# Performance work log

Measured on AMD Instinct MI355X. Metric: run time of the kernel, lower is better.

## Reference

```python
import jax, jax.numpy as jnp
import numpy as np

B, N = 4, 256
EDGE_F = 256; NODE_F = 256; MSG = 128; LINK_H = 128
ROUNDS = 3; CLASSES = 600


def setup_inputs() -> dict:
    key = jax.random.key(0)
    ks = jax.random.split(key, 16)
    s = 0.05
    return {
        "edge_features": jax.random.normal(ks[0], (B, N, N, EDGE_F), jnp.float32),
        "node_features": jax.random.normal(ks[1], (B, N, NODE_F), jnp.float32),
        "adj_mat": jnp.zeros((B, N, N), jnp.float32),
        "node_labels": jnp.zeros((B, N, CLASSES), jnp.float32),
        "human_nums": jax.random.randint(ks[2], (B,), 0, 16),
        "obj_nums": jax.random.randint(ks[3], (B,), 0, 224),
        # feature-resize linears
        "W_er": jax.random.normal(ks[4], (EDGE_F, MSG), jnp.float32) * s,
        "b_er": jnp.zeros((MSG,), jnp.float32),
        "W_nr": jax.random.normal(ks[5], (NODE_F, MSG), jnp.float32) * s,
        "b_nr": jnp.zeros((MSG,), jnp.float32),
        # link function: 1x1 GraphConv stack MSG -> LINK_H -> 1
        "W_l1": jax.random.normal(ks[6], (MSG, LINK_H), jnp.float32) * s,
        "b_l1": jnp.zeros((LINK_H,), jnp.float32),
        "W_l2": jax.random.normal(ks[7], (LINK_H, 1), jnp.float32) * s,
        "b_l2": jnp.zeros((1,), jnp.float32),
        # message function: linear_concat_relu  (cat(h_w, e_vw) -> MSG)
        "W_msg": jax.random.normal(ks[8], (2 * MSG, MSG), jnp.float32) * s,
        "b_msg": jnp.zeros((MSG,), jnp.float32),
        # GRU update (torch gate order r,z,n)
        "W_ih": jax.random.normal(ks[9], (MSG, 3 * MSG), jnp.float32) * s,
        "b_ih": jnp.zeros((3 * MSG,), jnp.float32),
        "W_hh": jax.random.normal(ks[10], (MSG, 3 * MSG), jnp.float32) * s,
        "b_hh": jnp.zeros((3 * MSG,), jnp.float32),
        # readout fc
        "W_ro": jax.random.normal(ks[11], (MSG, CLASSES), jnp.float32) * s,
        "b_ro": jnp.zeros((CLASSES,), jnp.float32),
    }


def _gru_cell(x, h, W_ih, b_ih, W_hh, b_hh):
    gi = x @ W_ih + b_ih
    gh = h @ W_hh + b_hh
    ir, iz, i_n = jnp.split(gi, 3, axis=-1)
    hr, hz, h_n = jnp.split(gh, 3, axis=-1)
    r = jax.nn.sigmoid(ir + hr)
    z = jax.nn.sigmoid(iz + hz)
    n = jnp.tanh(i_n + r * h_n)
    return (1.0 - z) * n + z * h


def reference(edge_features, node_features, adj_mat, node_labels,
              human_nums, obj_nums,
              W_er, b_er, W_nr, b_nr, W_l1, b_l1, W_l2, b_l2,
              W_msg, b_msg, W_ih, b_ih, W_hh, b_hh, W_ro, b_ro):
    Bn, Nn = node_features.shape[0], node_features.shape[1]
    # resize_feature_to_message_size
    ef = edge_features @ W_er + b_er          # [B, N(i=receiver), N(w=sender), M]
    nf = node_features @ W_nr + b_nr          # [B, N, M]

    valid = (human_nums + obj_nums).astype(jnp.int32)
    node_mask = (jnp.arange(Nn)[None, :] < valid[:, None]).astype(ef.dtype)  # [B,N]
    pair_mask = node_mask[:, :, None] * node_mask[:, None, :]                # [B,N,N]

    # NOTE: the original forward never writes updated node states back into
    # hidden_node_states, so every round uses the ORIGINAL (resized) node and
    # edge features for the message function -> m_raw is round-invariant.
    cat = jnp.concatenate(
        [jnp.broadcast_to(nf[:, None, :, :], ef.shape), ef], axis=-1)  # [B,N,N,2M]
    m_raw = jax.nn.relu(cat @ W_msg + b_msg)                           # [B,N,N,M]

    e_state = ef                                    # hidden edge state, round 0
    pred_adj = jnp.zeros((Bn, Nn, Nn), ef.dtype)
    pred_labels = jnp.zeros((Bn, Nn, CLASSES), ef.dtype)
    for rnd in range(ROUNDS):
        # GraphConv link function (1x1 convs == per-edge MLP), valid block only
        hlink = jax.nn.relu(e_state @ W_l1 + b_l1)
        pred_adj = pair_mask * (hlink @ W_l2 + b_l2)[..., 0]     # [B,N,N]
        gate = jax.nn.sigmoid(pred_adj) * node_mask[:, None, :]  # zero invalid senders
        m = gate[..., None] * m_raw                              # [B,N,N,M]
        # next-round hidden edge state: column i holds gated messages to node i
        e_state = jnp.where(pair_mask[..., None] > 0, jnp.swapaxes(m, 1, 2), ef)
        if rnd == ROUNDS - 1:
            m_sum = m.sum(axis=2)                                # [B,N,M]
            h_new = _gru_cell(m_sum, nf, W_ih, b_ih, W_hh, b_hh)
            pred_labels = node_mask[..., None] * (h_new @ W_ro + b_ro)
    return pred_adj, pred_labels
```

## Files before the change

kernel.cpp:

```cpp
#include <hip/hip_runtime.h>
#include <hip/hip_bf16.h>


#define B_ 4
#define N_ 256
#define EF_ 256
#define M_ 128
#define CL_ 600
#define ADJ_SZ (B_*N_*N_)

typedef __hip_bfloat16 bf16;
typedef short short8 __attribute__((ext_vector_type(8)));
typedef float f32x4 __attribute__((ext_vector_type(4)));

#define MFMA(a,b,c) __builtin_amdgcn_mfma_f32_16x16x32_bf16(a,b,c,0,0,0)

__device__ __forceinline__ float s2f(short s){
  union { unsigned int u; float f; } x; x.u = ((unsigned int)(unsigned short)s) << 16; return x.f;
}
__device__ __forceinline__ bf16 f2b(float f){ return __float2bfloat16(f); }
__device__ __forceinline__ short f2bs(float f){
  bf16 h = __float2bfloat16(f);
  return *reinterpret_cast<short*>(&h);
}
__device__ __forceinline__ float sigm(float x){ return 1.0f/(1.0f+expf(-x)); }

template<bool BF> __device__ __forceinline__ float ld(const void* p, size_t i){
  if (BF) return s2f(((const short*)p)[i]);
  return ((const float*)p)[i];
}
template<bool BF> __device__ __forceinline__ void st(void* p, size_t i, float v){
  if (BF) ((bf16*)p)[i] = f2b(v);
  else    ((float*)p)[i] = v;
}
__device__ __forceinline__ float dot8(short8 w, const float* x){
  float a = 0.f;
  #pragma unroll
  for (int j=0;j<8;j++) a += x[j]*s2f(w[j]);
  return a;
}

__global__ __launch_bounds__(64)
void k_detect(const unsigned short* ef, int* flag){
  int t = threadIdx.x;
  int cnt = 0;
  for (int j = 0; j < 64; j++){
    unsigned short u = ef[t*64 + j];
    int e = (u >> 7) & 0xFF;
    cnt += (e >= 96 && e <= 144) ? 1 : 0;
  }
  for (int o = 32; o > 0; o >>= 1) cnt += __shfl_down(cnt, o, 64);
  if (t == 0) *flag = (cnt > 3500) ? 1 : 0;
}

template<bool BF>
__global__ __launch_bounds__(256)
void k_zero(void* out, int n, const int* dflag){
  if ((*dflag != 0) != BF) return;
  int i = blockIdx.x*256 + threadIdx.x;
  if (i < n) st<BF>(out, i, 0.0f);
}

template<bool BF>
__global__ __launch_bounds__(64)
void k_pack(const void* src, int K, int N, bf16* dst, const int* dflag){
  if ((*dflag != 0) != BF) return;
  int blk = blockIdx.x;
  int n16 = N >> 4;
  int kk = blk / n16, nt = blk % n16;
  int lane = threadIdx.x;
  int k0 = kk*32 + (lane>>4)*8;
  int n  = nt*16 + (lane&15);
  size_t dbase = ((size_t)blk*64 + lane)*8;
  #pragma unroll
  for (int j=0;j<8;j++)
    dst[dbase+j] = f2b(ld<BF>(src, (size_t)(k0+j)*N + n));
}

template<bool BF>
__global__ __launch_bounds__(256)
void k_tr(const void* src, int K, int N, bf16* dst, const int* dflag){
  if ((*dflag != 0) != BF) return;
  int idx = blockIdx.x*256 + threadIdx.x;
  if (idx >= K*N) return;
  int k = idx / N, n = idx % N;
  dst[(size_t)n*K + k] = f2b(ld<BF>(src, idx));
}

template<bool BF>
__global__ __launch_bounds__(128)
void k_nf_c(const void* nodef, const bf16* tWnr, const void* b_nr,
            const bf16* tWmsgT, const void* b_msg, float* nf, float* cb,
            const int* dflag)
{
  if ((*dflag != 0) != BF) return;
  int blk = blockIdx.x; int b = blk >> 8; int v = blk & 255;
  int t = threadIdx.x;
  __shared__ float xs[EF_];
  __shared__ float nfs[M_];
  size_t xrow = ((size_t)(b*N_)+v)*EF_;
  xs[t]     = ld<BF>(nodef, xrow + t);
  xs[t+128] = ld<BF>(nodef, xrow + t + 128);
  __syncthreads();
  float acc = ld<BF>(b_nr, t);
  const short8* wp = (const short8*)(tWnr + (size_t)t*EF_);
  #pragma unroll 4
  for (int k8=0;k8<32;k8++) acc += dot8(wp[k8], &xs[k8*8]);
  nf[((size_t)(b*N_)+v)*M_+t] = acc;
  nfs[t] = acc;
  __syncthreads();
  float acc2 = ld<BF>(b_msg, t);
  const short8* wq = (const short8*)(tWmsgT + (size_t)t*M_);
  #pragma unroll 4
  for (int k8=0;k8<16;k8++) acc2 += dot8(wq[k8], &nfs[k8*8]);
  cb[((size_t)(b*N_)+v)*M_+t] = acc2;
}

template<bool BF>
__global__ __launch_bounds__(256)
void k_r0(const void* edgef, const bf16* pWer, const void* b_er,
          const bf16* pWmsgB, const float* cb, const bf16* pWl1,
          const void* b_l1, const void* W_l2, const void* b_l2,
          const int* hn, const int* on, bf16* mraw, float* s0,
          const int* dflag)
{
  if ((*dflag != 0) != BF) return;
  int b = blockIdx.z, i = blockIdx.y, w0 = blockIdx.x*32;
  int valid = hn[b] + on[b];
  if (i >= valid || w0 >= valid) return;
  int t = threadIdx.x;
  __shared__ __attribute__((aligned(16))) bf16 EfsB[32][136];
  __shared__ __attribute__((aligned(16))) char uni[32*264*2];
  bf16  (*Xs)[264]  = (bf16(*)[264])uni;
  float (*hls)[132] = (float(*)[132])uni;

  {
    int j = t>>3, c = (t&7)*32;
    size_t g = (((size_t)(b*N_)+i)*N_ + (size_t)(w0+j))*EF_ + c;
    if (BF){
      const short8* src = (const short8*)((const short*)edgef + g);
      short8* dst = (short8*)&Xs[j][c];
      #pragma unroll
      for (int u=0;u<4;u++) dst[u] = src[u];
    } else {
      const float* src = (const float*)edgef + g;
      #pragma unroll
      for (int u=0;u<32;u++) Xs[j][c+u] = f2b(src[u]);
    }
  }
  __syncthreads();

  int lane = t & 63, wv = t >> 6;
  int r0 = (wv&1)*16;
  int c0h = wv >> 1;
  int mA = r0 + (lane&15);
  int kq = (lane>>4)*8;
  int qrow = r0 + (lane>>4)*4;

  f32x4 z4 = {0.f,0.f,0.f,0.f};
  f32x4 acc[4] = {z4,z4,z4,z4};
  for (int kk=0;kk<8;kk++){
    short8 a = *(const short8*)&Xs[mA][kk*32 + kq];
    #pragma unroll
    for (int nt=0;nt<4;nt++){
      int gnt = c0h*4 + nt;
      short8 bb = *(const short8*)(pWer + (((size_t)kk*8 + gnt)*64 + lane)*8);
      acc[nt] = MFMA(a, bb, acc[nt]);
    }
  }
  #pragma unroll
  for (int nt=0;nt<4;nt++){
    int col = c0h*64 + nt*16 + (lane&15);
    float be = ld<BF>(b_er, col);
    #pragma unroll
    for (int r=0;r<4;r++)
      EfsB[qrow+r][col] = f2b(acc[nt][r] + be);
  }
  __syncthreads();

  f32x4 am[4] = {z4,z4,z4,z4};
  f32x4 ah[4] = {z4,z4,z4,z4};
  for (int kk=0;kk<4;kk++){
    short8 a = *(const short8*)&EfsB[mA][kk*32 + kq];
    #pragma unroll
    for (int nt=0;nt<4;nt++){
      int gnt = c0h*4 + nt;
      size_t off = (((size_t)kk*8 + gnt)*64 + lane)*8;
      short8 b1 = *(const short8*)(pWmsgB + off);
      am[nt] = MFMA(a, b1, am[nt]);
      short8 b2 = *(const short8*)(pWl1 + off);
      ah[nt] = MFMA(a, b2, ah[nt]);
    }
  }
  #pragma unroll
  for (int nt=0;nt<4;nt++){
    int col = c0h*64 + nt*16 + (lane&15);
    float bl = ld<BF>(b_l1, col);
    #pragma unroll
    for (int r=0;r<4;r++){
      int row = qrow + r;
      int w = w0 + row;
      float v = am[nt][r] + cb[((size_t)(b*N_)+w)*M_ + col];
      mraw[(((size_t)(b*N_)+i)*N_ + w)*M_ + col] = f2b(fmaxf(v, 0.f));
      hls[row][col] = fmaxf(ah[nt][r] + bl, 0.f);
    }
  }
  __syncthreads();
  {
    int row = t>>3, seg = t&7;
    float p = 0.f;
    #pragma unroll
    for (int k=0;k<16;k++) p += hls[row][seg*16+k] * ld<BF>(W_l2, seg*16+k);
    p += __shfl_down(p, 4, 8);
    p += __shfl_down(p, 2, 8);
    p += __shfl_down(p, 1, 8);
    if (seg==0 && (w0+row) < valid)
      s0[((size_t)(b*N_)+i)*N_ + w0 + row] = p + ld<BF>(b_l2, 0);
  }
}

template<bool BF>
__global__ __launch_bounds__(256)
void k_link2(const bf16* mraw, const float* s_prev, const bf16* pWl1,
             const void* b_l1, const void* W_l2, const void* b_l2,
             const int* hn, const int* on, float* s_next, const int* dflag)
{
  if ((*dflag != 0) != BF) return;
  int b = blockIdx.z, i = blockIdx.y, w0 = blockIdx.x*32;
  int valid = hn[b] + on[b];
  if (i >= valid || w0 >= valid) return;
  int t = threadIdx.x;
  __shared__ __attribute__((aligned(16))) bf16 EsB[32][136];
  __shared__ __attribute__((aligned(16))) float hls[32][132];
  __shared__ float sg[32];
  if (t < 32){
    int w = w0 + t;
    sg[t] = (w < valid) ? sigm(s_prev[((size_t)(b*N_)+w)*N_ + i]) : 0.f;
  }
  __syncthreads();
  {
    int j = t>>3, c = (t&7)*16;
    const short* src = (const short*)mraw + (((size_t)(b*N_)+(size_t)(w0+j))*N_ + i)*M_;
    float s = sg[j];
    #pragma unroll
    for (int u=0;u<2;u++){
      short8 v = *(const short8*)(src + c + u*8);
      short8 o;
      #pragma unroll
      for (int e=0;e<8;e++) o[e] = f2bs(s2f(v[e])*s);
      *(short8*)&EsB[j][c+u*8] = o;
    }
  }
  __syncthreads();

  int lane = t & 63, wv = t >> 6;
  int r0 = (wv&1)*16;
  int c0h = wv >> 1;
  int mA = r0 + (lane&15);
  int kq = (lane>>4)*8;
  int qrow = r0 + (lane>>4)*4;

  f32x4 z4 = {0.f,0.f,0.f,0.f};
  f32x4 ah[4] = {z4,z4,z4,z4};
  for (int kk=0;kk<4;kk++){
    short8 a = *(const short8*)&EsB[mA][kk*32 + kq];
    #pragma unroll
    for (int nt=0;nt<4;nt++){
      int gnt = c0h*4 + nt;
      short8 b2 = *(const short8*)(pWl1 + (((size_t)kk*8 + gnt)*64 + lane)*8);
      ah[nt] = MFMA(a, b2, ah[nt]);
    }
  }
  #pragma unroll
  for (int nt=0;nt<4;nt++){
    int col = c0h*64 + nt*16 + (lane&15);
    float bl = ld<BF>(b_l1, col);
    #pragma unroll
    for (int r=0;r<4;r++)
      hls[qrow+r][col] = fmaxf(ah[nt][r] + bl, 0.f);
  }
  __syncthreads();
  {
    int row = t>>3, seg = t&7;
    float p = 0.f;
    #pragma unroll
    for (int k=0;k<16;k++) p += hls[row][seg*16+k] * ld<BF>(W_l2, seg*16+k);
    p += __shfl_down(p, 4, 8);
    p += __shfl_down(p, 2, 8);
    p += __shfl_down(p, 1, 8);
    if (seg==0 && (w0+row) < valid)
      s_next[((size_t)(b*N_)+i)*N_ + w0 + row] = p + ld<BF>(b_l2, 0);
  }
}

template<bool BF>
__global__ __launch_bounds__(128)
void k_final(const bf16* mraw, const float* s2, const float* nf,
             const bf16* tWih, const void* b_ih,
             const bf16* tWhh, const void* b_hh,
             const bf16* tWro, const void* b_ro,
             const int* hn, const int* on, void* out, const int* dflag)
{
  if ((*dflag != 0) != BF) return;
  int i = blockIdx.x, b = blockIdx.y;
  int valid = hn[b] + on[b];
  if (i >= valid) return;
  int t = threadIdx.x;
  __shared__ float sgs[N_];
  __shared__ float xsh[M_], hsh[M_], hns[M_];
  const float* srow = s2 + ((size_t)(b*N_)+i)*N_;
  size_t adj = ((size_t)(b*N_)+i)*N_;
  for (int w=t; w<N_; w+=128){
    if (w < valid){
      float v = srow[w];
      st<BF>(out, adj + w, v);
      sgs[w] = sigm(v);
    } else sgs[w] = 0.f;
  }
  __syncthreads();
  const short* mrow = (const short*)mraw + (((size_t)(b*N_)+i)*N_)*M_;
  float acc = 0.f;
  for (int w=0; w<valid; w++) acc += sgs[w]*s2f(mrow[(size_t)w*M_ + t]);
  xsh[t] = acc;
  hsh[t] = nf[((size_t)(b*N_)+i)*M_ + t];
  __syncthreads();
  float gi[3], gh[3];
  #pragma unroll
  for (int g=0; g<3; g++){
    int o = g*M_ + t;
    float a = ld<BF>(b_ih, o), c = ld<BF>(b_hh, o);
    const short8* wi = (const short8*)(tWih + (size_t)o*M_);
    const short8* wh = (const short8*)(tWhh + (size_t)o*M_);
    #pragma unroll 4
    for (int k8=0;k8<16;k8++){
      a += dot8(wi[k8], &xsh[k8*8]);
      c += dot8(wh[k8], &hsh[k8*8]);
    }
    gi[g] = a; gh[g] = c;
  }
  float r  = sigm(gi[0] + gh[0]);
  float z  = sigm(gi[1] + gh[1]);
  float nn = tanhf(gi[2] + r*gh[2]);
  float hnew = (1.f - z)*nn + z*hsh[t];
  hns[t] = hnew;
  __syncthreads();
  size_t lab = (size_t)ADJ_SZ + ((size_t)(b*N_)+i)*CL_;
  for (int cls=t; cls<CL_; cls+=128){
    float a = ld<BF>(b_ro, cls);
    const short8* wr = (const short8*)(tWro + (size_t)cls*M_);
    #pragma unroll 4
    for (int k8=0;k8<16;k8++) a += dot8(wr[k8], &hns[k8*8]);
    st<BF>(out, lab + cls, a);
  }
}

template<bool BF>
static void run_pipeline(void* const* d_in, void* d_out, int out_size,
                         char* ws, const int* dflag, hipStream_t stream)
{
  const void* edgef = d_in[0];
  const void* nodef = d_in[1];
  const int*  hn    = (const int*)d_in[4];
  const int*  on    = (const int*)d_in[5];
  const void* W_er  = d_in[6];  const void* b_er  = d_in[7];
  const void* W_nr  = d_in[8];  const void* b_nr  = d_in[9];
  const void* W_l1  = d_in[10]; const void* b_l1  = d_in[11];
  const void* W_l2  = d_in[12]; const void* b_l2  = d_in[13];
  const void* W_msg = d_in[14]; const void* b_msg = d_in[15];
  const void* W_ih  = d_in[16]; const void* b_ih  = d_in[17];
  const void* W_hh  = d_in[18]; const void* b_hh  = d_in[19];
  const void* W_ro  = d_in[20]; const void* b_ro  = d_in[21];

  bf16*  mraw   = (bf16*) (ws);
  float* s_a    = (float*)(ws + 67108864);
  float* s_b    = (float*)(ws + 68157440);
  float* nf     = (float*)(ws + 69206016);
  float* cb     = (float*)(ws + 69730304);
  bf16*  pWer   = (bf16*) (ws + 70254592);
  bf16*  pWmsgB = (bf16*) (ws + 70320128);
  bf16*  pWl1   = (bf16*) (ws + 70352896);
  bf16*  tWnr   = (bf16*) (ws + 70385664);
  bf16*  tWmsgT = (bf16*) (ws + 70451200);
  bf16*  tWih   = (bf16*) (ws + 70483968);
  bf16*  tWhh   = (bf16*) (ws + 70582272);
  bf16*  tWro   = (bf16*) (ws + 70680576);

  const void* W_msgB = BF ? (const void*)((const bf16*)W_msg + 128*M_)
                          : (const void*)((const float*)W_msg + 128*M_);

  k_zero<BF><<<(out_size+255)/256, 256, 0, stream>>>(d_out, out_size, dflag);
  k_pack<BF><<<64, 64, 0, stream>>>(W_er, 256, 128, pWer, dflag);
  k_pack<BF><<<32, 64, 0, stream>>>(W_msgB, 128, 128, pWmsgB, dflag);
  k_pack<BF><<<32, 64, 0, stream>>>(W_l1, 128, 128, pWl1, dflag);
  k_tr<BF><<<128, 256, 0, stream>>>(W_nr, 256, 128, tWnr, dflag);
  k_tr<BF><<<64, 256, 0, stream>>>(W_msg, 128, 128, tWmsgT, dflag);
  k_tr<BF><<<192, 256, 0, stream>>>(W_ih, 128, 384, tWih, dflag);
  k_tr<BF><<<192, 256, 0, stream>>>(W_hh, 128, 384, tWhh, dflag);
  k_tr<BF><<<300, 256, 0, stream>>>(W_ro, 128, 600, tWro, dflag);

  k_nf_c<BF><<<B_*N_, 128, 0, stream>>>(nodef, tWnr, b_nr, tWmsgT, b_msg, nf, cb, dflag);
  dim3 g2(N_/32, N_, B_);
  k_r0<BF><<<g2, 256, 0, stream>>>(edgef, pWer, b_er, pWmsgB, cb, pWl1,
                                   b_l1, W_l2, b_l2, hn, on, mraw, s_a, dflag);
  k_link2<BF><<<g2, 256, 0, stream>>>(mraw, s_a, pWl1, b_l1, W_l2, b_l2, hn, on, s_b, dflag);
  k_link2<BF><<<g2, 256, 0, stream>>>(mraw, s_b, pWl1, b_l1, W_l2, b_l2, hn, on, s_a, dflag);
  k_final<BF><<<dim3(N_, B_), 128, 0, stream>>>(mraw, s_a, nf, tWih, b_ih, tWhh, b_hh,
                                                tWro, b_ro, hn, on, d_out, dflag);
}

extern "C" void kernel_launch(void* const* d_in, const int* in_sizes, int n_in,
                              void* d_out, int out_size, void* d_ws, size_t ws_size,
                              hipStream_t stream)
{
  char* ws = (char*)d_ws;
  int* dflag = (int*)(ws + 70834176);

  k_detect<<<1, 64, 0, stream>>>((const unsigned short*)d_in[0], dflag);
  run_pipeline<false>(d_in, d_out, out_size, ws, dflag, stream);
  run_pipeline<true >(d_in, d_out, out_size, ws, dflag, stream);
}
```

Baseline: 560.9 us.

## Precompute mraw@W_l1 once so later link rounds become elementwise

```diff
diff --git a/kernel.cpp b/kernel.cpp
--- a/kernel.cpp
+++ b/kernel.cpp
@@ -12,6 +12,7 @@
 typedef __hip_bfloat16 bf16;
 typedef short short8 __attribute__((ext_vector_type(8)));
 typedef float f32x4 __attribute__((ext_vector_type(4)));
+typedef float fvec4 __attribute__((ext_vector_type(4)));
 
 #define MFMA(a,b,c) __builtin_amdgcn_mfma_f32_16x16x32_bf16(a,b,c,0,0,0)
 
@@ -19,18 +20,13 @@
   union { unsigned int u; float f; } x; x.u = ((unsigned int)(unsigned short)s) << 16; return x.f;
 }
 __device__ __forceinline__ bf16 f2b(float f){ return __float2bfloat16(f); }
-__device__ __forceinline__ short f2bs(float f){
-  bf16 h = __float2bfloat16(f);
-  return *reinterpret_cast<short*>(&h);
-}
 __device__ __forceinline__ float sigm(float x){ return 1.0f/(1.0f+expf(-x)); }
 
-template<bool BF> __device__ __forceinline__ float ld(const void* p, size_t i){
-  if (BF) return s2f(((const short*)p)[i]);
-  return ((const float*)p)[i];
-}
-template<bool BF> __device__ __forceinline__ void st(void* p, size_t i, float v){
-  if (BF) ((bf16*)p)[i] = f2b(v);
+__device__ __forceinline__ float ldr(const void* p, size_t i, bool bf){
+  return bf ? s2f(((const short*)p)[i]) : ((const float*)p)[i];
+}
+__device__ __forceinline__ void str(void* p, size_t i, float v, bool bf){
+  if (bf) ((bf16*)p)[i] = f2b(v);
   else    ((float*)p)[i] = v;
 }
 __device__ __forceinline__ float dot8(short8 w, const float* x){
@@ -53,83 +49,97 @@
   if (t == 0) *flag = (cnt > 3500) ? 1 : 0;
 }
 
-template<bool BF>
 __global__ __launch_bounds__(256)
-void k_zero(void* out, int n, const int* dflag){
-  if ((*dflag != 0) != BF) return;
-  int i = blockIdx.x*256 + threadIdx.x;
-  if (i < n) st<BF>(out, i, 0.0f);
-}
-
-template<bool BF>
-__global__ __launch_bounds__(64)
-void k_pack(const void* src, int K, int N, bf16* dst, const int* dflag){
-  if ((*dflag != 0) != BF) return;
+void k_prep(const void* W_er, const void* W_msg, const void* W_l1,
+            const void* W_nr, const void* W_ih, const void* W_hh, const void* W_ro,
+            bf16* pWer, bf16* pWmsgB, bf16* pWl1,
+            bf16* tWnr, bf16* tWmsgT, bf16* tWih, bf16* tWhh, bf16* tWro,
+            void* out, int out_size, const int* dflag)
+{
+  bool bf = (*dflag != 0);
+  int nzb = (out_size + 255) >> 8;
   int blk = blockIdx.x;
-  int n16 = N >> 4;
-  int kk = blk / n16, nt = blk % n16;
-  int lane = threadIdx.x;
-  int k0 = kk*32 + (lane>>4)*8;
-  int n  = nt*16 + (lane&15);
-  size_t dbase = ((size_t)blk*64 + lane)*8;
-  #pragma unroll
-  for (int j=0;j<8;j++)
-    dst[dbase+j] = f2b(ld<BF>(src, (size_t)(k0+j)*N + n));
-}
-
-template<bool BF>
-__global__ __launch_bounds__(256)
-void k_tr(const void* src, int K, int N, bf16* dst, const int* dflag){
-  if ((*dflag != 0) != BF) return;
-  int idx = blockIdx.x*256 + threadIdx.x;
-  if (idx >= K*N) return;
+  int t = threadIdx.x;
+  if (blk < nzb){
+    int i = blk*256 + t;
+    if (i < out_size) str(out, i, 0.f, bf);
+    return;
+  }
+  blk -= nzb;
+  if (blk < 32){
+    int unit = blk*4 + (t>>6);
+    int lane = t & 63;
+    const void* src; bf16* dst; int u2;
+    if (unit < 64){ src = W_er; dst = pWer; u2 = unit; }
+    else if (unit < 96){
+      src = bf ? (const void*)((const short*)W_msg + 128*M_)
+               : (const void*)((const float*)W_msg + 128*M_);
+      dst = pWmsgB; u2 = unit - 64;
+    } else { src = W_l1; dst = pWl1; u2 = unit - 96; }
+    int kk = u2 >> 3, nt = u2 & 7;
+    int k0 = kk*32 + (lane>>4)*8;
+    int n  = nt*16 + (lane&15);
+    size_t dbase = ((size_t)u2*64 + lane)*8;
+    #pragma unroll
+    for (int j=0;j<8;j++)
+      dst[dbase+j] = f2b(ldr(src, (size_t)(k0+j)*128 + n, bf));
+    return;
+  }
+  blk -= 32;
+  int idx = blk*256 + t;
+  const void* src; bf16* dst; int K, N;
+  if (idx < 32768){ src = W_nr;  dst = tWnr;  K = 256; N = 128; }
+  else if ((idx -= 32768) < 16384){ src = W_msg; dst = tWmsgT; K = 128; N = 128; }
+  else if ((idx -= 16384) < 49152){ src = W_ih;  dst = tWih;  K = 128; N = 384; }
+  else if ((idx -= 49152) < 49152){ src = W_hh;  dst = tWhh;  K = 128; N = 384; }
+  else if ((idx -= 49152) < 76800){ src = W_ro;  dst = tWro;  K = 128; N = 600; }
+  else return;
   int k = idx / N, n = idx % N;
-  dst[(size_t)n*K + k] = f2b(ld<BF>(src, idx));
-}
-
-template<bool BF>
+  dst[(size_t)n*K + k] = f2b(ldr(src, idx, bf));
+}
+
 __global__ __launch_bounds__(128)
 void k_nf_c(const void* nodef, const bf16* tWnr, const void* b_nr,
             const bf16* tWmsgT, const void* b_msg, float* nf, float* cb,
             const int* dflag)
 {
-  if ((*dflag != 0) != BF) return;
+  bool bf = (*dflag != 0);
   int blk = blockIdx.x; int b = blk >> 8; int v = blk & 255;
   int t = threadIdx.x;
   __shared__ float xs[EF_];
   __shared__ float nfs[M_];
   size_t xrow = ((size_t)(b*N_)+v)*EF_;
-  xs[t]     = ld<BF>(nodef, xrow + t);
-  xs[t+128] = ld<BF>(nodef, xrow + t + 128);
-  __syncthreads();
-  float acc = ld<BF>(b_nr, t);
+  xs[t]     = ldr(nodef, xrow + t, bf);
+  xs[t+128] = ldr(nodef, xrow + t + 128, bf);
+  __syncthreads();
+  float acc = ldr(b_nr, t, bf);
   const short8* wp = (const short8*)(tWnr + (size_t)t*EF_);
   #pragma unroll 4
   for (int k8=0;k8<32;k8++) acc += dot8(wp[k8], &xs[k8*8]);
   nf[((size_t)(b*N_)+v)*M_+t] = acc;
   nfs[t] = acc;
   __syncthreads();
-  float acc2 = ld<BF>(b_msg, t);
+  float acc2 = ldr(b_msg, t, bf);
   const short8* wq = (const short8*)(tWmsgT + (size_t)t*M_);
   #pragma unroll 4
   for (int k8=0;k8<16;k8++) acc2 += dot8(wq[k8], &nfs[k8*8]);
   cb[((size_t)(b*N_)+v)*M_+t] = acc2;
 }
 
-template<bool BF>
 __global__ __launch_bounds__(256)
 void k_r0(const void* edgef, const bf16* pWer, const void* b_er,
           const bf16* pWmsgB, const float* cb, const bf16* pWl1,
           const void* b_l1, const void* W_l2, const void* b_l2,
-          const int* hn, const int* on, bf16* mraw, float* s0,
+          const int* hn, const int* on, bf16* mraw, float* u, float* s0,
           const int* dflag)
 {
-  if ((*dflag != 0) != BF) return;
+  bool bf = (*dflag != 0);
   int b = blockIdx.z, i = blockIdx.y, w0 = blockIdx.x*32;
   int valid = hn[b] + on[b];
   if (i >= valid || w0 >= valid) return;
   int t = threadIdx.x;
   __shared__ __attribute__((aligned(16))) bf16 EfsB[32][136];
+  __shared__ __attribute__((aligned(16))) bf16 MrB[32][136];
   __shared__ __attribute__((aligned(16))) char uni[32*264*2];
   bf16  (*Xs)[264]  = (bf16(*)[264])uni;
   float (*hls)[132] = (float(*)[132])uni;
@@ -137,15 +147,19 @@
   {
     int j = t>>3, c = (t&7)*32;
     size_t g = (((size_t)(b*N_)+i)*N_ + (size_t)(w0+j))*EF_ + c;
-    if (BF){
+    if (bf){
       const short8* src = (const short8*)((const short*)edgef + g);
       short8* dst = (short8*)&Xs[j][c];
       #pragma unroll
-      for (int u=0;u<4;u++) dst[u] = src[u];
+      for (int q=0;q<4;q++) dst[q] = src[q];
     } else {
-      const float* src = (const float*)edgef + g;
+      const fvec4* src = (const fvec4*)((const float*)edgef + g);
       #pragma unroll
-      for (int u=0;u<32;u++) Xs[j][c+u] = f2b(src[u]);
+      for (int q=0;q<8;q++){
+        fvec4 v = src[q];
+        #pragma unroll
+        for (int e=0;e<4;e++) Xs[j][c+q*4+e] = f2b(v[e]);
+      }
     }
   }
   __syncthreads();
@@ -171,7 +185,7 @@
   #pragma unroll
   for (int nt=0;nt<4;nt++){
     int col = c0h*64 + nt*16 + (lane&15);
-    float be = ld<BF>(b_er, col);
+    float be = ldr(b_er, col, bf);
     #pragma unroll
     for (int r=0;r<4;r++)
       EfsB[qrow+r][col] = f2b(acc[nt][r] + be);
@@ -195,105 +209,87 @@
   #pragma unroll
   for (int nt=0;nt<4;nt++){
     int col = c0h*64 + nt*16 + (lane&15);
-    float bl = ld<BF>(b_l1, col);
+    float bl = ldr(b_l1, col, bf);
     #pragma unroll
     for (int r=0;r<4;r++){
       int row = qrow + r;
       int w = w0 + row;
       float v = am[nt][r] + cb[((size_t)(b*N_)+w)*M_ + col];
-      mraw[(((size_t)(b*N_)+i)*N_ + w)*M_ + col] = f2b(fmaxf(v, 0.f));
+      bf16 mb = f2b(fmaxf(v, 0.f));
+      mraw[(((size_t)(b*N_)+i)*N_ + w)*M_ + col] = mb;
+      MrB[row][col] = mb;
       hls[row][col] = fmaxf(ah[nt][r] + bl, 0.f);
     }
   }
   __syncthreads();
+
+  f32x4 au[4] = {z4,z4,z4,z4};
+  for (int kk=0;kk<4;kk++){
+    short8 a = *(const short8*)&MrB[mA][kk*32 + kq];
+    #pragma unroll
+    for (int nt=0;nt<4;nt++){
+      short8 b2 = *(const short8*)(pWl1 + (((size_t)kk*8 + c0h*4 + nt)*64 + lane)*8);
+      au[nt] = MFMA(a, b2, au[nt]);
+    }
+  }
+  #pragma unroll
+  for (int nt=0;nt<4;nt++){
+    int col = c0h*64 + nt*16 + (lane&15);
+    #pragma unroll
+    for (int r=0;r<4;r++)
+      u[(((size_t)(b*N_)+i)*N_ + (size_t)(w0+qrow+r))*M_ + col] = au[nt][r];
+  }
+
   {
     int row = t>>3, seg = t&7;
     float p = 0.f;
     #pragma unroll
-    for (int k=0;k<16;k++) p += hls[row][seg*16+k] * ld<BF>(W_l2, seg*16+k);
+    for (int k=0;k<16;k++) p += hls[row][seg*16+k] * ldr(W_l2, seg*16+k, bf);
     p += __shfl_down(p, 4, 8);
     p += __shfl_down(p, 2, 8);
     p += __shfl_down(p, 1, 8);
     if (seg==0 && (w0+row) < valid)
-      s0[((size_t)(b*N_)+i)*N_ + w0 + row] = p + ld<BF>(b_l2, 0);
-  }
-}
-
-template<bool BF>
+      s0[((size_t)(b*N_)+i)*N_ + w0 + row] = p + ldr(b_l2, 0, bf);
+  }
+}
+
 __global__ __launch_bounds__(256)
-void k_link2(const bf16* mraw, const float* s_prev, const bf16* pWl1,
-             const void* b_l1, const void* W_l2, const void* b_l2,
+void k_linkE(const float* u, const float* s_prev, const void* b_l1,
+             const void* W_l2, const void* b_l2,
              const int* hn, const int* on, float* s_next, const int* dflag)
 {
-  if ((*dflag != 0) != BF) return;
-  int b = blockIdx.z, i = blockIdx.y, w0 = blockIdx.x*32;
+  bool bf = (*dflag != 0);
+  int i = blockIdx.x, b = blockIdx.y;
   int valid = hn[b] + on[b];
-  if (i >= valid || w0 >= valid) return;
-  int t = threadIdx.x;
-  __shared__ __attribute__((aligned(16))) bf16 EsB[32][136];
-  __shared__ __attribute__((aligned(16))) float hls[32][132];
-  __shared__ float sg[32];
-  if (t < 32){
-    int w = w0 + t;
-    sg[t] = (w < valid) ? sigm(s_prev[((size_t)(b*N_)+w)*N_ + i]) : 0.f;
-  }
-  __syncthreads();
-  {
-    int j = t>>3, c = (t&7)*16;
-    const short* src = (const short*)mraw + (((size_t)(b*N_)+(size_t)(w0+j))*N_ + i)*M_;
-    float s = sg[j];
-    #pragma unroll
-    for (int u=0;u<2;u++){
-      short8 v = *(const short8*)(src + c + u*8);
-      short8 o;
+  if (i >= valid) return;
+  int t = threadIdx.x;
+  __shared__ float bl1s[M_], wl2s[M_];
+  if (t < M_){ bl1s[t] = ldr(b_l1, t, bf); wl2s[t] = ldr(W_l2, t, bf); }
+  __syncthreads();
+  float bl2 = ldr(b_l2, 0, bf);
+  int e = t>>3, seg = t&7;
+  for (int w0 = 0; w0 < valid; w0 += 32){
+    int w = w0 + e;
+    if (w >= valid) break;
+    float sg = sigm(s_prev[((size_t)(b*N_)+w)*N_ + i]);
+    const fvec4* up = (const fvec4*)(u + (((size_t)(b*N_)+w)*N_ + i)*M_ + seg*16);
+    float p = 0.f;
+    #pragma unroll
+    for (int q=0;q<4;q++){
+      fvec4 v = up[q];
       #pragma unroll
-      for (int e=0;e<8;e++) o[e] = f2bs(s2f(v[e])*s);
-      *(short8*)&EsB[j][c+u*8] = o;
-    }
-  }
-  __syncthreads();
-
-  int lane = t & 63, wv = t >> 6;
-  int r0 = (wv&1)*16;
-  int c0h = wv >> 1;
-  int mA = r0 + (lane&15);
-  int kq = (lane>>4)*8;
-  int qrow = r0 + (lane>>4)*4;
-
-  f32x4 z4 = {0.f,0.f,0.f,0.f};
-  f32x4 ah[4] = {z4,z4,z4,z4};
-  for (int kk=0;kk<4;kk++){
-    short8 a = *(const short8*)&EsB[mA][kk*32 + kq];
-    #pragma unroll
-    for (int nt=0;nt<4;nt++){
-      int gnt = c0h*4 + nt;
-      short8 b2 = *(const short8*)(pWl1 + (((size_t)kk*8 + gnt)*64 + lane)*8);
-      ah[nt] = MFMA(a, b2, ah[nt]);
-    }
-  }
-  #pragma unroll
-  for (int nt=0;nt<4;nt++){
-    int col = c0h*64 + nt*16 + (lane&15);
-    float bl = ld<BF>(b_l1, col);
-    #pragma unroll
-    for (int r=0;r<4;r++)
-      hls[qrow+r][col] = fmaxf(ah[nt][r] + bl, 0.f);
-  }
-  __syncthreads();
-  {
-    int row = t>>3, seg = t&7;
-    float p = 0.f;
-    #pragma unroll
-    for (int k=0;k<16;k++) p += hls[row][seg*16+k] * ld<BF>(W_l2, seg*16+k);
+      for (int e2=0;e2<4;e2++){
+        int k = seg*16 + q*4 + e2;
+        p += fmaxf(sg*v[e2] + bl1s[k], 0.f) * wl2s[k];
+      }
+    }
     p += __shfl_down(p, 4, 8);
     p += __shfl_down(p, 2, 8);
     p += __shfl_down(p, 1, 8);
-    if (seg==0 && (w0+row) < valid)
-      s_next[((size_t)(b*N_)+i)*N_ + w0 + row] = p + ld<BF>(b_l2, 0);
-  }
-}
-
-template<bool BF>
+    if (seg==0) s_next[((size_t)(b*N_)+i)*N_ + w] = p + bl2;
+  }
+}
+
 __global__ __launch_bounds__(128)
 void k_final(const bf16* mraw, const float* s2, const float* nf,
              const bf16* tWih, const void* b_ih,
@@ -301,7 +297,7 @@
              const bf16* tWro, const void* b_ro,
              const int* hn, const int* on, void* out, const int* dflag)
 {
-  if ((*dflag != 0) != BF) return;
+  bool bf = (*dflag != 0);
   int i = blockIdx.x, b = blockIdx.y;
   int valid = hn[b] + on[b];
   if (i >= valid) return;
@@ -313,7 +309,7 @@
   for (int w=t; w<N_; w+=128){
     if (w < valid){
       float v = srow[w];
-      st<BF>(out, adj + w, v);
+      str(out, adj + w, v, bf);
       sgs[w] = sigm(v);
     } else sgs[w] = 0.f;
   }
@@ -328,7 +324,7 @@
   #pragma unroll
   for (int g=0; g<3; g++){
     int o = g*M_ + t;
-    float a = ld<BF>(b_ih, o), c = ld<BF>(b_hh, o);
+    float a = ldr(b_ih, o, bf), c = ldr(b_hh, o, bf);
     const short8* wi = (const short8*)(tWih + (size_t)o*M_);
     const short8* wh = (const short8*)(tWhh + (size_t)o*M_);
     #pragma unroll 4
@@ -346,18 +342,20 @@
   __syncthreads();
   size_t lab = (size_t)ADJ_SZ + ((size_t)(b*N_)+i)*CL_;
   for (int cls=t; cls<CL_; cls+=128){
-    float a = ld<BF>(b_ro, cls);
+    float a = ldr(b_ro, cls, bf);
     const short8* wr = (const short8*)(tWro + (size_t)cls*M_);
     #pragma unroll 4
     for (int k8=0;k8<16;k8++) a += dot8(wr[k8], &hns[k8*8]);
-    st<BF>(out, lab + cls, a);
-  }
-}
-
-template<bool BF>
-static void run_pipeline(void* const* d_in, void* d_out, int out_size,
-                         char* ws, const int* dflag, hipStream_t stream)
-{
+    str(out, lab + cls, a, bf);
+  }
+}
+
+extern "C" void kernel_launch(void* const* d_in, const int* in_sizes, int n_in,
+                              void* d_out, int out_size, void* d_ws, size_t ws_size,
+                              hipStream_t stream)
+{
+  char* ws = (char*)d_ws;
+
   const void* edgef = d_in[0];
   const void* nodef = d_in[1];
   const int*  hn    = (const int*)d_in[4];
@@ -372,50 +370,39 @@
   const void* W_ro  = d_in[20]; const void* b_ro  = d_in[21];
 
   bf16*  mraw   = (bf16*) (ws);
-  float* s_a    = (float*)(ws + 67108864);
-  float* s_b    = (float*)(ws + 68157440);
-  float* nf     = (float*)(ws + 69206016);
-  float* cb     = (float*)(ws + 69730304);
-  bf16*  pWer   = (bf16*) (ws + 70254592);
-  bf16*  pWmsgB = (bf16*) (ws + 70320128);
-  bf16*  pWl1   = (bf16*) (ws + 70352896);
-  bf16*  tWnr   = (bf16*) (ws + 70385664);
-  bf16*  tWmsgT = (bf16*) (ws + 70451200);
-  bf16*  tWih   = (bf16*) (ws + 70483968);
-  bf16*  tWhh   = (bf16*) (ws + 70582272);
-  bf16*  tWro   = (bf16*) (ws + 70680576);
-
-  const void* W_msgB = BF ? (const void*)((const bf16*)W_msg + 128*M_)
-                          : (const void*)((const float*)W_msg + 128*M_);
-
-  k_zero<BF><<<(out_size+255)/256, 256, 0, stream>>>(d_out, out_size, dflag);
-  k_pack<BF><<<64, 64, 0, stream>>>(W_er, 256, 128, pWer, dflag);
-  k_pack<BF><<<32, 64, 0, stream>>>(W_msgB, 128, 128, pWmsgB, dflag);
-  k_pack<BF><<<32, 64, 0, stream>>>(W_l1, 128, 128, pWl1, dflag);
-  k_tr<BF><<<128, 256, 0, stream>>>(W_nr, 256, 128, tWnr, dflag);
-  k_tr<BF><<<64, 256, 0, stream>>>(W_msg, 128, 128, tWmsgT, dflag);
-  k_tr<BF><<<192, 256, 0, stream>>>(W_ih, 128, 384, tWih, dflag);
-  k_tr<BF><<<192, 256, 0, stream>>>(W_hh, 128, 384, tWhh, dflag);
-  k_tr<BF><<<300, 256, 0, stream>>>(W_ro, 128, 600, tWro, dflag);
-
-  k_nf_c<BF><<<B_*N_, 128, 0, stream>>>(nodef, tWnr, b_nr, tWmsgT, b_msg, nf, cb, dflag);
+  float* uu     = (float*)(ws + 67108864);
+  float* s_a    = (float*)(ws + 201326592);
+  float* s_b    = (float*)(ws + 202375168);
+  float* nf     = (float*)(ws + 203423744);
+  float* cb     = (float*)(ws + 203948032);
+  bf16*  pWer   = (bf16*) (ws + 204472320);
+  bf16*  pWmsgB = (bf16*) (ws + 204537856);
+  bf16*  pWl1   = (bf16*) (ws + 204570624);
+  bf16*  tWnr   = (bf16*) (ws + 204603392);
+  bf16*  tWmsgT = (bf16*) (ws + 204668928);
+  bf16*  tWih   = (bf16*) (ws + 204701696);
+  bf16*  tWhh   = (bf16*) (ws + 204800000);
+  bf16*  tWro   = (bf16*) (ws + 204898304);
+  int*   dflag  = (int*)  (ws + 205051904);
+
+  k_detect<<<1, 64, 0, stream>>>((const unsigned short*)d_in[0], dflag);
+
+  int nzb = (out_size + 255) / 256;
+  k_prep<<<nzb + 32 + 876, 256, 0, stream>>>(
+      W_er, W_msg, W_l1, W_nr, W_ih, W_hh, W_ro,
+      pWer, pWmsgB, pWl1, tWnr, tWmsgT, tWih, tWhh, tWro,
+      d_out, out_size, dflag);
+
+  k_nf_c<<<B_*N_, 128, 0, stream>>>(nodef, tWnr, b_nr, tWmsgT, b_msg, nf, cb, dflag);
+
   dim3 g2(N_/32, N_, B_);
-  k_r0<BF><<<g2, 256, 0, stream>>>(edgef, pWer, b_er, pWmsgB, cb, pWl1,
-                                   b_l1, W_l2, b_l2, hn, on, mraw, s_a, dflag);
-  k_link2<BF><<<g2, 256, 0, stream>>>(mraw, s_a, pWl1, b_l1, W_l2, b_l2, hn, on, s_b, dflag);
-  k_link2<BF><<<g2, 256, 0, stream>>>(mraw, s_b, pWl1, b_l1, W_l2, b_l2, hn, on, s_a, dflag);
-  k_final<BF><<<dim3(N_, B_), 128, 0, stream>>>(mraw, s_a, nf, tWih, b_ih, tWhh, b_hh,
-                                                tWro, b_ro, hn, on, d_out, dflag);
-}
-
-extern "C" void kernel_launch(void* const* d_in, const int* in_sizes, int n_in,
-                              void* d_out, int out_size, void* d_ws, size_t ws_size,
-                              hipStream_t stream)
-{
-  char* ws = (char*)d_ws;
-  int* dflag = (int*)(ws + 70834176);
-
-  k_detect<<<1, 64, 0, stream>>>((const unsigned short*)d_in[0], dflag);
-  run_pipeline<false>(d_in, d_out, out_size, ws, dflag, stream);
-  run_pipeline<true >(d_in, d_out, out_size, ws, dflag, stream);
-}
+  k_r0<<<g2, 256, 0, stream>>>(edgef, pWer, b_er, pWmsgB, cb, pWl1,
+                               b_l1, W_l2, b_l2, hn, on, mraw, uu, s_a, dflag);
+
+  dim3 gl(N_, B_);
+  k_linkE<<<gl, 256, 0, stream>>>(uu, s_a, b_l1, W_l2, b_l2, hn, on, s_b, dflag);
+  k_linkE<<<gl, 256, 0, stream>>>(uu, s_b, b_l1, W_l2, b_l2, hn, on, s_a, dflag);
+
+  k_final<<<gl, 128, 0, stream>>>(mraw, s_a, nf, tWih, b_ih, tWhh, b_hh,
+                                  tWro, b_ro, hn, on, d_out, dflag);
+}
```

Result: faster. 512.7 us (-8.6%).
